# Kernel tuning notes

Hardware: AMD Instinct MI355X
Metric: run time of the kernel (lower is better)

The kernel has to match this reference:

```python
import jax, jax.numpy as jnp
import numpy as np

# Config (matches init_kwargs)
LOW_T = 100      # low_res_timesteps
HIGH_T = 2000    # high_res_timesteps
FEAT = 6         # feature_dim
HID = 256        # student_hidden_dim
NUM_CLASSES = 10
LBL_DIM = 16
UP = HIGH_T // LOW_T  # upsampling_factor = 20
B = 4096


def setup_inputs() -> dict:
    key = jax.random.key(0)
    ks = jax.random.split(key, 20)

    def lin(k, fan_in, fan_out):
        # torch nn.Linear default init: U(-1/sqrt(fan_in), 1/sqrt(fan_in))
        kw, kb = jax.random.split(k)
        bound = 1.0 / np.sqrt(fan_in)
        W = jax.random.uniform(kw, (fan_in, fan_out), jnp.float32, -bound, bound)
        b = jax.random.uniform(kb, (fan_out,), jnp.float32, -bound, bound)
        return W, b

    W1, b1 = lin(ks[0], LOW_T * FEAT, HID * 2)
    W2, b2 = lin(ks[1], HID * 2, HID)
    W3, b3 = lin(ks[2], HID, HID // 2)
    dec_in = HID // 2 + LBL_DIM
    W4, b4 = lin(ks[3], dec_in, HID)
    W5, b5 = lin(ks[4], HID, HID * 2)
    W6, b6 = lin(ks[5], HID * 2, HIGH_T * FEAT)
    emb = jax.random.normal(ks[6], (NUM_CLASSES, LBL_DIM), jnp.float32)

    low_res_data = jax.random.normal(ks[7], (B, LOW_T, FEAT), jnp.float32)
    labels = jax.random.randint(ks[8], (B,), 0, NUM_CLASSES, jnp.int64)
    return {
        'low_res_data': low_res_data, 'labels': labels,
        'W1': W1, 'b1': b1, 'W2': W2, 'b2': b2, 'W3': W3, 'b3': b3,
        'W4': W4, 'b4': b4, 'W5': W5, 'b5': b5, 'W6': W6, 'b6': b6,
        'emb': emb,
    }


def reference(low_res_data, labels, W1, b1, W2, b2, W3, b3, W4, b4, W5, b5, W6, b6, emb):
    batch = low_res_data.shape[0]
    # Encoder MLP (dropout is identity in eval mode)
    x = low_res_data.reshape(batch, -1)                     # [B, LOW_T*FEAT]
    h = jax.nn.relu(x @ W1 + b1)
    h = jax.nn.relu(h @ W2 + b2)
    feat = h @ W3 + b3                                      # [B, HID//2]
    # Label conditioning
    feat = jnp.concatenate([feat, emb[labels]], axis=-1)    # [B, HID//2 + LBL_DIM]
    # Decoder MLP
    h = jax.nn.relu(feat @ W4 + b4)
    h = jax.nn.relu(h @ W5 + b5)
    decoded = (h @ W6 + b6).reshape(batch, HIGH_T, FEAT)    # [B, H, F]

    # Vectorized constraint enforcement + smoothing (replaces per-timestep python loop):
    #  - at anchor timesteps t = i*UP: output = low_res_data[:, i]
    #  - between anchors i and i+1: lin = (1-a)*low[i] + a*low[i+1];
    #      out = lin + 0.2 * (decoded - lin)
    #  - after the last anchor interval ((LOW_T-1)*UP < t < HIGH_T): out = decoded
    t = jnp.arange(HIGH_T)
    seg = jnp.clip(t // UP, 0, LOW_T - 2)                   # segment index per timestep
    alpha = ((t - seg * UP) / UP).astype(decoded.dtype)     # [H], 0 at anchors, 1 at seg end
    start = low_res_data[:, seg]                            # [B, H, F]
    end = low_res_data[:, seg + 1]                          # [B, H, F]
    a = alpha[None, :, None]
    lin_interp = (1.0 - a) * start + a * end                # equals low point at anchors
    blend = lin_interp + 0.2 * (decoded - lin_interp)
    is_anchor = (t % UP == 0)[None, :, None]
    in_interior = (t < (LOW_T - 1) * UP)[None, :, None]
    enhanced = jnp.where(is_anchor, lin_interp, jnp.where(in_interior, blend, decoded))
    return enhanced
```

## Files before the change

### kernel.cpp

```cpp
#include <hip/hip_runtime.h>
#include <hip/hip_bf16.h>

typedef __attribute__((ext_vector_type(8))) short bf16x8;
typedef __attribute__((ext_vector_type(4))) float f32x4;
typedef __attribute__((ext_vector_type(8))) unsigned short u16x8;
typedef unsigned short ushort_t;
typedef unsigned int u32;

__device__ __forceinline__ ushort_t f2b(float f) {
    u32 u = __builtin_bit_cast(u32, f);
    u += 0x7FFFu + ((u >> 16) & 1u);
    return (ushort_t)(u >> 16);
}

__device__ __forceinline__ void gload_lds16(const void* g, void* l) {
    __builtin_amdgcn_global_load_lds(
        (const __attribute__((address_space(1))) u32*)g,
        (__attribute__((address_space(3))) u32*)l, 16, 0, 0);
}

struct TrDesc { const float* src; ushort_t* dst; int K, N, Kpad, Npad, base, nx; };
struct TrArgs { TrDesc d[6]; const float* low; ushort_t* xb; int trbase; };

__global__ __launch_bounds__(256) void prep_kernel(TrArgs a) {
    const int bid = blockIdx.x, tid = threadIdx.x;
    if (bid >= a.trbase) {
        int idx = (bid - a.trbase) * 256 + tid;
        int b = idx / 76, c = idx - b * 76;
        ushort_t* dp = a.xb + (size_t)b * 608 + c * 8;
        u16x8 o;
        if (c < 75) {
            const float* sp = a.low + (size_t)b * 600 + c * 8;
            f32x4 v0 = *(const f32x4*)sp, v1 = *(const f32x4*)(sp + 4);
            #pragma unroll
            for (int j = 0; j < 4; ++j) { o[j] = f2b(v0[j]); o[4 + j] = f2b(v1[j]); }
        } else {
            #pragma unroll
            for (int j = 0; j < 8; ++j) o[j] = 0;
        }
        *(u16x8*)dp = o;
        return;
    }
    __shared__ float T[64][65];
    int w = 0;
    #pragma unroll
    for (int i = 1; i < 6; ++i) if (bid >= a.d[i].base) w = i;
    const TrDesc d = a.d[w];
    const int local = bid - d.base;
    const int n0 = (local % d.nx) * 64, k0 = (local / d.nx) * 64;
    #pragma unroll
    for (int it = 0; it < 16; ++it) {
        int idx = it * 256 + tid;
        int r = idx >> 6, c = idx & 63;
        int k = k0 + r, n = n0 + c;
        T[c][r] = (k < d.K && n < d.N) ? d.src[(size_t)k * d.N + n] : 0.f;
    }
    __syncthreads();
    #pragma unroll
    for (int it = 0; it < 16; ++it) {
        int idx = it * 256 + tid;
        int r = idx >> 6, c = idx & 63;
        int n = n0 + r, k = k0 + c;
        if (k < d.Kpad)
            d.dst[(size_t)n * d.Kpad + k] = f2b(T[r][c]);
    }
}

template<int EPI>
__global__ __launch_bounds__(256, 4) void gemm64(
    const ushort_t* __restrict__ A, const ushort_t* __restrict__ Bt,
    const float* __restrict__ bias, ushort_t* __restrict__ Cb,
    const int* __restrict__ lbl, const float* __restrict__ emb,
    int K, int Nreal, int ldc)
{
    __shared__ ushort_t As[2][64 * 32];
    __shared__ ushort_t Bs[2][64 * 32];
    const int tid = threadIdx.x;
    const int wave = tid >> 6, lane = tid & 63;
    const int l15 = lane & 15, g = lane >> 4;
    const int wr = wave >> 1, wc = wave & 1;
    const int m0 = blockIdx.y * 64, n0 = blockIdx.x * 64;

    f32x4 acc[2][2] = {};

    const int p0 = tid * 16;
    const int row0 = p0 >> 6;
    const int k0s = (((p0 & 63) ^ (((row0 >> 1) & 3) << 4)) >> 1);
    const ushort_t* a0 = A + (size_t)(m0 + row0) * K + k0s;
    const ushort_t* b0 = Bt + (size_t)(n0 + row0) * K + k0s;

    char* AsB = (char*)As + wave * 1024;
    char* BsB = (char*)Bs + wave * 1024;

    const int sxor = ((l15 >> 1) & 3) << 4;
    const ushort_t* ardA = &As[0][0] + (((wr * 32 + l15) * 64 + ((g * 16) ^ sxor)) >> 1);
    const ushort_t* brdB = &Bs[0][0] + (((wc * 32 + l15) * 64 + ((g * 16) ^ sxor)) >> 1);

    const int nk = K >> 5;
    gload_lds16(a0, AsB); gload_lds16(b0, BsB);
    a0 += 32; b0 += 32;
    __syncthreads();
    #pragma unroll 2
    for (int kk = 0; kk < nk; ++kk) {
        const int cur = kk & 1, nxt = cur ^ 1;
        if (kk + 1 < nk) {
            gload_lds16(a0, AsB + nxt * 4096);
            gload_lds16(b0, BsB + nxt * 4096);
            a0 += 32; b0 += 32;
        }
        bf16x8 af[2], bf[2];
        #pragma unroll
        for (int i = 0; i < 2; ++i) af[i] = *(const bf16x8*)(ardA + cur * 2048 + i * 512);
        #pragma unroll
        for (int j = 0; j < 2; ++j) bf[j] = *(const bf16x8*)(brdB + cur * 2048 + j * 512);
        #pragma unroll
        for (int i = 0; i < 2; ++i)
            #pragma unroll
            for (int j = 0; j < 2; ++j)
                acc[i][j] = __builtin_amdgcn_mfma_f32_16x16x32_bf16(af[i], bf[j], acc[i][j], 0, 0, 0);
        __syncthreads();
    }

    #pragma unroll
    for (int i = 0; i < 2; ++i)
        #pragma unroll
        for (int r = 0; r < 4; ++r) {
            int row = m0 + wr * 32 + i * 16 + g * 4 + r;
            #pragma unroll
            for (int j = 0; j < 2; ++j) {
                int col = n0 + wc * 32 + j * 16 + l15;
                if (col >= Nreal) continue;
                float v = acc[i][j][r] + bias[col];
                if (EPI == 0) v = fmaxf(v, 0.f);
                Cb[(size_t)row * ldc + col] = f2b(v);
            }
        }

    if (EPI == 1 && blockIdx.x == 0) {
        #pragma unroll
        for (int q = 0; q < 8; ++q) {
            int e = tid + q * 256;
            int row = m0 + (e >> 5), c = e & 31;
            float v = c < 16 ? emb[(size_t)lbl[row] * 16 + c] : 0.f;
            Cb[(size_t)row * ldc + 128 + c] = f2b(v);
        }
    }
}

__global__ __launch_bounds__(256, 4) void gemm128_l6(
    const ushort_t* __restrict__ A, const ushort_t* __restrict__ Bt,
    const float* __restrict__ bias, float* __restrict__ Cf,
    const float* __restrict__ low, int K)
{
    __shared__ ushort_t As[2][128 * 32];
    __shared__ ushort_t Bs[2][128 * 32];
    const int tid = threadIdx.x;
    const int wave = tid >> 6, lane = tid & 63;
    const int l15 = lane & 15, g = lane >> 4;
    const int wr = wave >> 1, wc = wave & 1;
    const int m0 = blockIdx.y * 128, n0 = blockIdx.x * 128;

    f32x4 acc[4][4] = {};

    const int p0 = tid * 16;
    const int row0 = p0 >> 6;
    const int k0s = (((p0 & 63) ^ (((row0 >> 1) & 3) << 4)) >> 1);
    const int p1 = 4096 + tid * 16;
    const int row1 = p1 >> 6;
    const int k1s = (((p1 & 63) ^ (((row1 >> 1) & 3) << 4)) >> 1);

    const ushort_t* a0 = A + (size_t)(m0 + row0) * K + k0s;
    const ushort_t* a1 = A + (size_t)(m0 + row1) * K + k1s;
    const ushort_t* b0 = Bt + (size_t)(n0 + row0) * K + k0s;
    const ushort_t* b1 = Bt + (size_t)(n0 + row1) * K + k1s;

    char* AsB = (char*)As + wave * 1024;
    char* BsB = (char*)Bs + wave * 1024;

    const int sxor = ((l15 >> 1) & 3) << 4;
    const ushort_t* ardA = &As[0][0] + (((wr * 64 + l15) * 64 + ((g * 16) ^ sxor)) >> 1);
    const ushort_t* brdB = &Bs[0][0] + (((wc * 64 + l15) * 64 + ((g * 16) ^ sxor)) >> 1);

    const int nk = K >> 5;
    gload_lds16(a0, AsB); gload_lds16(a1, AsB + 4096);
    gload_lds16(b0, BsB); gload_lds16(b1, BsB + 4096);
    a0 += 32; a1 += 32; b0 += 32; b1 += 32;
    __syncthreads();
    #pragma unroll 2
    for (int kk = 0; kk < nk; ++kk) {
        const int cur = kk & 1, nxt = cur ^ 1;
        if (kk + 1 < nk) {
            gload_lds16(a0, AsB + nxt * 8192);
            gload_lds16(a1, AsB + nxt * 8192 + 4096);
            gload_lds16(b0, BsB + nxt * 8192);
            gload_lds16(b1, BsB + nxt * 8192 + 4096);
            a0 += 32; a1 += 32; b0 += 32; b1 += 32;
        }
        bf16x8 af[4], bf[4];
        #pragma unroll
        for (int i = 0; i < 4; ++i) af[i] = *(const bf16x8*)(ardA + cur * 4096 + i * 512);
        #pragma unroll
        for (int j = 0; j < 4; ++j) bf[j] = *(const bf16x8*)(brdB + cur * 4096 + j * 512);
        #pragma unroll
        for (int i = 0; i < 4; ++i)
            #pragma unroll
            for (int j = 0; j < 4; ++j)
                acc[i][j] = __builtin_amdgcn_mfma_f32_16x16x32_bf16(af[i], bf[j], acc[i][j], 0, 0, 0);
        __syncthreads();
    }

    float bvv[4]; int offv[4]; float alphav[4];
    bool anch[4], interi[4], valid[4];
    #pragma unroll
    for (int j = 0; j < 4; ++j) {
        int col = n0 + wc * 64 + j * 16 + l15;
        valid[j] = col < 12000;
        int cc = valid[j] ? col : 0;
        bvv[j] = bias[cc];
        int t = cc / 6, f = cc - t * 6;
        int seg = t / 20; if (seg > 98) seg = 98;
        offv[j] = seg * 6 + f;
        alphav[j] = (float)(t - seg * 20) * 0.05f;
        anch[j] = (t % 20) == 0;
        interi[j] = t < 1980;
    }
    const int colb = n0 + wc * 64 + l15;
    #pragma unroll
    for (int i = 0; i < 4; ++i)
        #pragma unroll
        for (int r = 0; r < 4; ++r) {
            const int row = m0 + wr * 64 + i * 16 + g * 4 + r;
            const float* lrow = low + (size_t)row * 600;
            float* orow = Cf + (size_t)row * 12000;
            #pragma unroll
            for (int j = 0; j < 4; ++j) {
                if (!valid[j]) continue;
                float s = lrow[offv[j]], e = lrow[offv[j] + 6];
                float lin = (1.f - alphav[j]) * s + alphav[j] * e;
                float dec = acc[i][j][r] + bvv[j];
                float res = anch[j] ? lin : (interi[j] ? lin + 0.2f * (dec - lin) : dec);
                __builtin_nontemporal_store(res, &orow[colb + j * 16]);
            }
        }
}

extern "C" void kernel_launch(void* const* d_in, const int* in_sizes, int n_in,
                              void* d_out, int out_size, void* d_ws, size_t ws_size,
                              hipStream_t stream) {
    const float* low = (const float*)d_in[0];
    const int*   lbl = (const int*)d_in[1];
    const float* W1 = (const float*)d_in[2];  const float* b1 = (const float*)d_in[3];
    const float* W2 = (const float*)d_in[4];  const float* b2 = (const float*)d_in[5];
    const float* W3 = (const float*)d_in[6];  const float* b3 = (const float*)d_in[7];
    const float* W4 = (const float*)d_in[8];  const float* b4 = (const float*)d_in[9];
    const float* W5 = (const float*)d_in[10]; const float* b5 = (const float*)d_in[11];
    const float* W6 = (const float*)d_in[12]; const float* b6 = (const float*)d_in[13];
    const float* emb = (const float*)d_in[14];
    float* out = (float*)d_out;

    char* ws = (char*)d_ws;
    size_t off = 0;
    auto alloc = [&](size_t elems) {
        ushort_t* p = (ushort_t*)(ws + off);
        off = (off + elems * 2 + 255) & ~(size_t)255;
        return p;
    };
    ushort_t* xb  = alloc((size_t)4096 * 608);
    ushort_t* w1t = alloc((size_t)512 * 608);
    ushort_t* w2t = alloc((size_t)256 * 512);
    ushort_t* w3t = alloc((size_t)128 * 256);
    ushort_t* w4t = alloc((size_t)256 * 160);
    ushort_t* w5t = alloc((size_t)512 * 256);
    ushort_t* w6t = alloc((size_t)12032 * 512);
    ushort_t* h1  = alloc((size_t)4096 * 512);
    ushort_t* h2  = alloc((size_t)4096 * 256);
    ushort_t* fc  = alloc((size_t)4096 * 160);
    ushort_t* h4  = alloc((size_t)4096 * 256);
    ushort_t* h5  = alloc((size_t)4096 * 512);

    TrArgs ta;
    int base = 0;
    auto mk = [&](int i, const float* s, ushort_t* d, int K, int N, int Kp, int Np) {
        int nx = Np / 64, ny = (Kp + 63) / 64;
        ta.d[i] = TrDesc{s, d, K, N, Kp, Np, base, nx};
        base += nx * ny;
    };
    mk(0, W1, w1t, 600, 512, 608, 512);
    mk(1, W2, w2t, 512, 256, 512, 256);
    mk(2, W3, w3t, 256, 128, 256, 128);
    mk(3, W4, w4t, 144, 256, 160, 256);
    mk(4, W5, w5t, 256, 512, 256, 512);
    mk(5, W6, w6t, 512, 12000, 512, 12032);
    ta.low = low; ta.xb = xb; ta.trbase = base;
    const int castx_blocks = (4096 * 76) / 256;

    prep_kernel<<<dim3(base + castx_blocks), 256, 0, stream>>>(ta);

    gemm64<0><<<dim3(8, 64), 256, 0, stream>>>(xb, w1t, b1, h1, nullptr, nullptr, 608, 512, 512);
    gemm64<0><<<dim3(4, 64), 256, 0, stream>>>(h1, w2t, b2, h2, nullptr, nullptr, 512, 256, 256);
    gemm64<1><<<dim3(2, 64), 256, 0, stream>>>(h2, w3t, b3, fc, lbl, emb, 256, 128, 160);
    gemm64<0><<<dim3(4, 64), 256, 0, stream>>>(fc, w4t, b4, h4, nullptr, nullptr, 160, 256, 256);
    gemm64<0><<<dim3(8, 64), 256, 0, stream>>>(h4, w5t, b5, h5, nullptr, nullptr, 256, 512, 512);
    gemm128_l6<<<dim3(94, 32), 256, 0, stream>>>(h5, w6t, b6, out, low, 512);
}
```

Before: 392.0 us.

## Fuse five encoder/decoder GEMMs into one persistent chain kernel with LDS-resident activations

Replaces the five separate layer GEMM launches, and the input cast pass, with a single kernel. Each block owns 16 rows and keeps their activations in shared memory across layers 1-5, streaming weights in double-buffered tiles and writing only h5 to global memory. This removes launch overhead and the global round-trips for intermediate activations, but each block re-reads every weight matrix and uses only 256 blocks of 16-row MFMA work. It also switches the final output stores from nontemporal to regular stores.

```diff
diff --git a/kernel.cpp b/kernel.cpp
--- a/kernel.cpp
+++ b/kernel.cpp
@@ -20,28 +20,11 @@
 }
 
 struct TrDesc { const float* src; ushort_t* dst; int K, N, Kpad, Npad, base, nx; };
-struct TrArgs { TrDesc d[6]; const float* low; ushort_t* xb; int trbase; };
+struct TrArgs { TrDesc d[6]; };
 
 __global__ __launch_bounds__(256) void prep_kernel(TrArgs a) {
+    __shared__ float T[64][65];
     const int bid = blockIdx.x, tid = threadIdx.x;
-    if (bid >= a.trbase) {
-        int idx = (bid - a.trbase) * 256 + tid;
-        int b = idx / 76, c = idx - b * 76;
-        ushort_t* dp = a.xb + (size_t)b * 608 + c * 8;
-        u16x8 o;
-        if (c < 75) {
-            const float* sp = a.low + (size_t)b * 600 + c * 8;
-            f32x4 v0 = *(const f32x4*)sp, v1 = *(const f32x4*)(sp + 4);
-            #pragma unroll
-            for (int j = 0; j < 4; ++j) { o[j] = f2b(v0[j]); o[4 + j] = f2b(v1[j]); }
-        } else {
-            #pragma unroll
-            for (int j = 0; j < 8; ++j) o[j] = 0;
-        }
-        *(u16x8*)dp = o;
-        return;
-    }
-    __shared__ float T[64][65];
     int w = 0;
     #pragma unroll
     for (int i = 1; i < 6; ++i) if (bid >= a.d[i].base) w = i;
@@ -66,84 +49,122 @@
     }
 }
 
-template<int EPI>
-__global__ __launch_bounds__(256, 4) void gemm64(
-    const ushort_t* __restrict__ A, const ushort_t* __restrict__ Bt,
-    const float* __restrict__ bias, ushort_t* __restrict__ Cb,
-    const int* __restrict__ lbl, const float* __restrict__ emb,
-    int K, int Nreal, int ldc)
+__device__ __forceinline__ void layer_run(
+    const char* actIn, char* actOut, char* Bsb,
+    const ushort_t* __restrict__ Wt, const float* __restrict__ bias,
+    int K, int N, bool relu, int tid)
 {
-    __shared__ ushort_t As[2][64 * 32];
-    __shared__ ushort_t Bs[2][64 * 32];
-    const int tid = threadIdx.x;
     const int wave = tid >> 6, lane = tid & 63;
     const int l15 = lane & 15, g = lane >> 4;
-    const int wr = wave >> 1, wc = wave & 1;
-    const int m0 = blockIdx.y * 64, n0 = blockIdx.x * 64;
-
-    f32x4 acc[2][2] = {};
-
-    const int p0 = tid * 16;
-    const int row0 = p0 >> 6;
-    const int k0s = (((p0 & 63) ^ (((row0 >> 1) & 3) << 4)) >> 1);
-    const ushort_t* a0 = A + (size_t)(m0 + row0) * K + k0s;
-    const ushort_t* b0 = Bt + (size_t)(n0 + row0) * K + k0s;
-
-    char* AsB = (char*)As + wave * 1024;
-    char* BsB = (char*)Bs + wave * 1024;
-
+    const int row_t = tid >> 2;
+    const int sw_s = ((row_t >> 1) & 3) << 4;
+    const int koff = ((((tid & 3) << 4)) ^ sw_s) >> 1;
     const int sxor = ((l15 >> 1) & 3) << 4;
-    const ushort_t* ardA = &As[0][0] + (((wr * 32 + l15) * 64 + ((g * 16) ^ sxor)) >> 1);
-    const ushort_t* brdB = &Bs[0][0] + (((wc * 32 + l15) * 64 + ((g * 16) ^ sxor)) >> 1);
-
+    const int aRd = l15 * 64 + ((g * 16) ^ sxor);
+    const int bRd = wave * 4096 + l15 * 64 + ((g * 16) ^ sxor);
+    char* stW = Bsb + wave * 1024;
     const int nk = K >> 5;
-    gload_lds16(a0, AsB); gload_lds16(b0, BsB);
-    a0 += 32; b0 += 32;
-    __syncthreads();
-    #pragma unroll 2
-    for (int kk = 0; kk < nk; ++kk) {
-        const int cur = kk & 1, nxt = cur ^ 1;
-        if (kk + 1 < nk) {
-            gload_lds16(a0, AsB + nxt * 4096);
-            gload_lds16(b0, BsB + nxt * 4096);
-            a0 += 32; b0 += 32;
-        }
-        bf16x8 af[2], bf[2];
-        #pragma unroll
-        for (int i = 0; i < 2; ++i) af[i] = *(const bf16x8*)(ardA + cur * 2048 + i * 512);
-        #pragma unroll
-        for (int j = 0; j < 2; ++j) bf[j] = *(const bf16x8*)(brdB + cur * 2048 + j * 512);
-        #pragma unroll
-        for (int i = 0; i < 2; ++i)
-            #pragma unroll
-            for (int j = 0; j < 2; ++j)
-                acc[i][j] = __builtin_amdgcn_mfma_f32_16x16x32_bf16(af[i], bf[j], acc[i][j], 0, 0, 0);
+    const int nmt = (N + 255) >> 8;
+
+    for (int mt = 0; mt < nmt; ++mt) {
+        const int ncols = N - mt * 256;
+        const ushort_t* src0 = Wt + (size_t)(mt * 256 + row_t) * K + koff;
+        f32x4 acc[4] = {};
+        #pragma unroll
+        for (int i = 0; i < 4; ++i)
+            if (i * 64 < ncols) gload_lds16(src0 + (size_t)i * 64 * K, stW + i * 4096);
         __syncthreads();
-    }
-
-    #pragma unroll
-    for (int i = 0; i < 2; ++i)
-        #pragma unroll
-        for (int r = 0; r < 4; ++r) {
-            int row = m0 + wr * 32 + i * 16 + g * 4 + r;
-            #pragma unroll
-            for (int j = 0; j < 2; ++j) {
-                int col = n0 + wc * 32 + j * 16 + l15;
-                if (col >= Nreal) continue;
-                float v = acc[i][j][r] + bias[col];
-                if (EPI == 0) v = fmaxf(v, 0.f);
-                Cb[(size_t)row * ldc + col] = f2b(v);
+        for (int kk = 0; kk < nk; ++kk) {
+            const int cur = kk & 1, nxt = cur ^ 1;
+            if (kk + 1 < nk) {
+                #pragma unroll
+                for (int i = 0; i < 4; ++i)
+                    if (i * 64 < ncols)
+                        gload_lds16(src0 + (size_t)i * 64 * K + (kk + 1) * 32,
+                                    stW + nxt * 16384 + i * 4096);
             }
-        }
-
-    if (EPI == 1 && blockIdx.x == 0) {
-        #pragma unroll
-        for (int q = 0; q < 8; ++q) {
-            int e = tid + q * 256;
-            int row = m0 + (e >> 5), c = e & 31;
-            float v = c < 16 ? emb[(size_t)lbl[row] * 16 + c] : 0.f;
-            Cb[(size_t)row * ldc + 128 + c] = f2b(v);
-        }
+            bf16x8 af = *(const bf16x8*)(actIn + kk * 1024 + aRd);
+            #pragma unroll
+            for (int j = 0; j < 4; ++j) {
+                bf16x8 bf = *(const bf16x8*)(Bsb + cur * 16384 + bRd + j * 1024);
+                acc[j] = __builtin_amdgcn_mfma_f32_16x16x32_bf16(af, bf, acc[j], 0, 0, 0);
+            }
+            __syncthreads();
+        }
+        #pragma unroll
+        for (int j = 0; j < 4; ++j) {
+            int col = mt * 256 + wave * 64 + j * 16 + l15;
+            if (col < N) {
+                float bv = bias[col];
+                #pragma unroll
+                for (int r = 0; r < 4; ++r) {
+                    float v = acc[j][r] + bv;
+                    if (relu) v = fmaxf(v, 0.f);
+                    int mrow = g * 4 + r;
+                    int sw = ((mrow >> 1) & 3) << 4;
+                    *(ushort_t*)(actOut + (col >> 5) * 1024 + mrow * 64 +
+                                 ((2 * (col & 31)) ^ sw)) = f2b(v);
+                }
+            }
+        }
+    }
+    __syncthreads();
+}
+
+struct ChainArgs {
+    const float* low; const int* lbl; const float* emb;
+    const ushort_t *w1t, *w2t, *w3t, *w4t, *w5t;
+    const float *b1, *b2, *b3, *b4, *b5;
+    ushort_t* h5;
+};
+
+__global__ __launch_bounds__(256) void chain_kernel(ChainArgs a) {
+    __shared__ __align__(16) char smem[19456 + 16384 + 2 * 16384];
+    char* act0 = smem;
+    char* act1 = smem + 19456;
+    char* Bsb  = smem + 19456 + 16384;
+    const int tid = threadIdx.x;
+    const int m0 = blockIdx.x << 4;
+
+    for (int u = tid; u < 1216; u += 256) {
+        int row = u / 76, c8 = u - row * 76;
+        int sw = ((row >> 1) & 3) << 4;
+        char* dst = act0 + (c8 >> 2) * 1024 + row * 64 + ((((c8 & 3) << 4)) ^ sw);
+        u16x8 o;
+        if (c8 < 75) {
+            const float* sp = a.low + (size_t)(m0 + row) * 600 + c8 * 8;
+            f32x4 v0 = *(const f32x4*)sp, v1 = *(const f32x4*)(sp + 4);
+            #pragma unroll
+            for (int j = 0; j < 4; ++j) { o[j] = f2b(v0[j]); o[4 + j] = f2b(v1[j]); }
+        } else {
+            #pragma unroll
+            for (int j = 0; j < 8; ++j) o[j] = 0;
+        }
+        *(u16x8*)dst = o;
+    }
+    __syncthreads();
+
+    layer_run(act0, act1, Bsb, a.w1t, a.b1, 608, 512, true,  tid);
+    layer_run(act1, act0, Bsb, a.w2t, a.b2, 512, 256, true,  tid);
+    layer_run(act0, act1, Bsb, a.w3t, a.b3, 256, 128, false, tid);
+
+    for (int u = tid; u < 512; u += 256) {
+        int row = u >> 5, c = u & 31;
+        float v = c < 16 ? a.emb[(size_t)a.lbl[m0 + row] * 16 + c] : 0.f;
+        int sw = ((row >> 1) & 3) << 4;
+        *(ushort_t*)(act1 + 4096 + row * 64 + ((2 * c) ^ sw)) = f2b(v);
+    }
+    __syncthreads();
+
+    layer_run(act1, act0, Bsb, a.w4t, a.b4, 160, 256, true, tid);
+    layer_run(act0, act1, Bsb, a.w5t, a.b5, 256, 512, true, tid);
+
+    for (int u = tid; u < 1024; u += 256) {
+        int row = u >> 6, c8 = u & 63;
+        int sw = ((row >> 1) & 3) << 4;
+        u16x8 v = *(const u16x8*)(act1 + (c8 >> 2) * 1024 + row * 64 +
+                                  (((c8 & 3) << 4) ^ sw));
+        *(u16x8*)(a.h5 + (size_t)(m0 + row) * 512 + (c8 << 3)) = v;
     }
 }
 
@@ -239,7 +260,7 @@
                 float lin = (1.f - alphav[j]) * s + alphav[j] * e;
                 float dec = acc[i][j][r] + bvv[j];
                 float res = anch[j] ? lin : (interi[j] ? lin + 0.2f * (dec - lin) : dec);
-                __builtin_nontemporal_store(res, &orow[colb + j * 16]);
+                orow[colb + j * 16] = res;
             }
         }
 }
@@ -265,17 +286,12 @@
         off = (off + elems * 2 + 255) & ~(size_t)255;
         return p;
     };
-    ushort_t* xb  = alloc((size_t)4096 * 608);
     ushort_t* w1t = alloc((size_t)512 * 608);
     ushort_t* w2t = alloc((size_t)256 * 512);
     ushort_t* w3t = alloc((size_t)128 * 256);
     ushort_t* w4t = alloc((size_t)256 * 160);
     ushort_t* w5t = alloc((size_t)512 * 256);
     ushort_t* w6t = alloc((size_t)12032 * 512);
-    ushort_t* h1  = alloc((size_t)4096 * 512);
-    ushort_t* h2  = alloc((size_t)4096 * 256);
-    ushort_t* fc  = alloc((size_t)4096 * 160);
-    ushort_t* h4  = alloc((size_t)4096 * 256);
     ushort_t* h5  = alloc((size_t)4096 * 512);
 
     TrArgs ta;
@@ -291,15 +307,15 @@
     mk(3, W4, w4t, 144, 256, 160, 256);
     mk(4, W5, w5t, 256, 512, 256, 512);
     mk(5, W6, w6t, 512, 12000, 512, 12032);
-    ta.low = low; ta.xb = xb; ta.trbase = base;
-    const int castx_blocks = (4096 * 76) / 256;
-
-    prep_kernel<<<dim3(base + castx_blocks), 256, 0, stream>>>(ta);
-
-    gemm64<0><<<dim3(8, 64), 256, 0, stream>>>(xb, w1t, b1, h1, nullptr, nullptr, 608, 512, 512);
-    gemm64<0><<<dim3(4, 64), 256, 0, stream>>>(h1, w2t, b2, h2, nullptr, nullptr, 512, 256, 256);
-    gemm64<1><<<dim3(2, 64), 256, 0, stream>>>(h2, w3t, b3, fc, lbl, emb, 256, 128, 160);
-    gemm64<0><<<dim3(4, 64), 256, 0, stream>>>(fc, w4t, b4, h4, nullptr, nullptr, 160, 256, 256);
-    gemm64<0><<<dim3(8, 64), 256, 0, stream>>>(h4, w5t, b5, h5, nullptr, nullptr, 256, 512, 512);
+
+    prep_kernel<<<dim3(base), 256, 0, stream>>>(ta);
+
+    ChainArgs ca;
+    ca.low = low; ca.lbl = lbl; ca.emb = emb;
+    ca.w1t = w1t; ca.w2t = w2t; ca.w3t = w3t; ca.w4t = w4t; ca.w5t = w5t;
+    ca.b1 = b1; ca.b2 = b2; ca.b3 = b3; ca.b4 = b4; ca.b5 = b5;
+    ca.h5 = h5;
+    chain_kernel<<<dim3(256), 256, 0, stream>>>(ca);
+
     gemm128_l6<<<dim3(94, 32), 256, 0, stream>>>(h5, w6t, b6, out, low, 512);
 }
```

Result: faster. 380.9 us (-2.8%).
